# Kernel tuning notes

Hardware: AMD Instinct MI355X
Metric: run time of the kernel (lower is better)

The kernel has to match this reference:

```python
import jax, jax.numpy as jnp
import numpy as np

B, H, W, C = 16, 32, 32, 512
HEADS, DHEAD = 8, 64  # head * channel == C
GROUPS, EPS = 32, 1e-5


def setup_inputs() -> dict:
    key = jax.random.key(0)
    ks = jax.random.split(key, 6)
    return {
        "x": jax.random.normal(ks[0], (B, H, W, C), jnp.float32),
        "gn_gamma": jnp.ones((C,), jnp.float32),
        "gn_beta": jnp.zeros((C,), jnp.float32),
        "wq": jax.random.normal(ks[1], (C, HEADS * DHEAD), jnp.float32) * 0.02,
        "wk": jax.random.normal(ks[2], (C, HEADS * DHEAD), jnp.float32) * 0.02,
        "wv": jax.random.normal(ks[3], (C, HEADS * DHEAD), jnp.float32) * 0.02,
        "conv_w": jax.random.normal(ks[4], (3, 3, HEADS * DHEAD, C), jnp.float32) * 0.02,
        "conv_b": jnp.zeros((C,), jnp.float32),
    }


def _group_norm(x, gamma, beta):
    b, h, w, c = x.shape
    xg = x.reshape(b, h, w, GROUPS, c // GROUPS)
    mean = jnp.mean(xg, axis=(1, 2, 4), keepdims=True)
    var = jnp.var(xg, axis=(1, 2, 4), keepdims=True)
    xn = (xg - mean) * jax.lax.rsqrt(var + EPS)
    return xn.reshape(b, h, w, c) * gamma + beta


def reference(x, gn_gamma, gn_beta, wq, wk, wv, conv_w, conv_b):
    xn = _group_norm(x, gn_gamma, gn_beta)          # [B,H,W,C]
    t = xn.reshape(B, H * W, C)                      # tokens [B,S,C]
    q = (t @ wq).reshape(B, H * W, HEADS, DHEAD)
    k = (t @ wk).reshape(B, H * W, HEADS, DHEAD)
    v = (t @ wv).reshape(B, H * W, HEADS, DHEAD)
    scale = 1.0 / jnp.sqrt(jnp.asarray(DHEAD, q.dtype))
    scores = jnp.einsum("bqhd,bkhd->bhqk", q, k) * scale  # [B,HEADS,S,S]
    weights = jax.nn.softmax(scores, axis=-1)
    out = jnp.einsum("bhqk,bkhd->bqhd", weights, v)       # [B,S,HEADS,DHEAD]
    out = out.reshape(B, H, W, HEADS * DHEAD)
    y = jax.lax.conv_general_dilated(
        out, conv_w, window_strides=(1, 1), padding=((1, 1), (1, 1)),
        dimension_numbers=("NHWC", "HWIO", "NHWC")) + conv_b
    return y + x
```

## Files before the change

### kernel.cpp

```cpp
#include <hip/hip_runtime.h>
#include <hip/hip_bf16.h>

#define Bn 16
#define Cc 512
#define Ss 1024
#define HEADS 8
#define DHEAD 64
#define GROUPS 32
#define CPG 16
#define EPSv 1e-5f
#define Mtok (Bn*Ss)
#define QKVS 1536
#define QKS 1024
#define PROW 34
#define PIMG (PROW*PROW)

typedef __hip_bfloat16 bf16;
typedef __attribute__((ext_vector_type(8))) short short8;
typedef __attribute__((ext_vector_type(4))) float f32x4;

union U4 { uint4 u; bf16 h[8]; };
union B4 { ushort4 u; bf16 h[4]; };

__device__ __forceinline__ void stage16(const bf16* g, bf16* l) {
    __builtin_amdgcn_global_load_lds((const __attribute__((address_space(1))) void*)g,
                                     (__attribute__((address_space(3))) void*)l,
                                     16, 0, 0);
}

__device__ __forceinline__ unsigned int pkbf(float a, float b) {
    union { __hip_bfloat16 h; unsigned short u; } ua, ub;
    ua.h = __float2bfloat16(a); ub.h = __float2bfloat16(b);
    return ((unsigned int)ub.u << 16) | ua.u;
}

__device__ __forceinline__ void swz_decode(int F, int& r, int& c) {
    int line = F >> 3, pos = F & 7;
    int u = pos ^ (line & 7);
    r = (line << 1) | (u >> 2);
    c = u & 3;
}
__device__ __forceinline__ int swz_off(int r, int q) {
    return (r >> 1) * 64 + (((((r & 1) << 2) + q) ^ ((r >> 1) & 7)) << 3);
}

__global__ __launch_bounds__(256) void wtrans(const float* __restrict__ src,
                                              bf16* __restrict__ dst) {
    size_t off = (size_t)blockIdx.y * 262144;
    int t = blockIdx.x * 256 + threadIdx.x;
    int n = t & 511, k8 = (t >> 9) * 8;
    const float* s = src + off + (size_t)k8 * 512 + n;
    U4 o;
#pragma unroll
    for (int j = 0; j < 8; j++) o.h[j] = __float2bfloat16(s[(size_t)j * 512]);
    *(uint4*)(dst + off + (size_t)n * 512 + k8) = o.u;
}

__global__ __launch_bounds__(256) void gn_stats(const float* __restrict__ x,
                                                float* __restrict__ stats) {
    int bg = blockIdx.x;
    int b = bg >> 5, g = bg & 31;
    int tid = threadIdx.x;
    const size_t base = (size_t)b * Ss * Cc + g * CPG;
    float sum = 0.f, sq = 0.f;
    for (int i = tid; i < 4096; i += 256) {
        int s = i >> 2, c4 = (i & 3) * 4;
        float4 t = *(const float4*)(x + base + (size_t)s * Cc + c4);
        sum += t.x + t.y + t.z + t.w;
        sq  += t.x * t.x + t.y * t.y + t.z * t.z + t.w * t.w;
    }
    __shared__ float s1[4], s2[4];
#pragma unroll
    for (int off = 32; off > 0; off >>= 1) {
        sum += __shfl_down(sum, off);
        sq  += __shfl_down(sq,  off);
    }
    if ((tid & 63) == 0) { s1[tid >> 6] = sum; s2[tid >> 6] = sq; }
    __syncthreads();
    if (tid == 0) {
        float S = s1[0] + s1[1] + s1[2] + s1[3];
        float Q = s2[0] + s2[1] + s2[2] + s2[3];
        float mean = S * (1.f / 16384.f);
        float var  = Q * (1.f / 16384.f) - mean * mean;
        stats[bg * 2 + 0] = mean;
        stats[bg * 2 + 1] = rsqrtf(var + EPSv);
    }
}

__global__ __launch_bounds__(256) void gn_apply(const float* __restrict__ x,
                                                const float* __restrict__ stats,
                                                const float* __restrict__ gamma,
                                                const float* __restrict__ beta,
                                                bf16* __restrict__ xn) {
    size_t i = (size_t)blockIdx.x * 256 + threadIdx.x;
    size_t e = i * 4;
    int c0 = (int)(e & (Cc - 1));
    int token = (int)(e >> 9);
    int b = token >> 10;
    int g = c0 >> 4;
    float mean = stats[(b * 32 + g) * 2 + 0];
    float rstd = stats[(b * 32 + g) * 2 + 1];
    float4 t  = *(const float4*)(x + e);
    float4 gm = *(const float4*)(gamma + c0);
    float4 bt = *(const float4*)(beta + c0);
    B4 o;
    o.h[0] = __float2bfloat16((t.x - mean) * rstd * gm.x + bt.x);
    o.h[1] = __float2bfloat16((t.y - mean) * rstd * gm.y + bt.y);
    o.h[2] = __float2bfloat16((t.z - mean) * rstd * gm.z + bt.z);
    o.h[3] = __float2bfloat16((t.w - mean) * rstd * gm.w + bt.w);
    *(ushort4*)(xn + e) = o.u;
}

__global__ __launch_bounds__(256) void zero_pad(bf16* __restrict__ Pad) {
    int idx = blockIdx.x * 256 + threadIdx.x;
    int b = idx / (132 * 64);
    int rem = idx - b * 132 * 64;
    int t = rem >> 6, seg = rem & 63;
    int r, c;
    if (t < 34)      { r = 0;  c = t; }
    else if (t < 68) { r = 33; c = t - 34; }
    else { int u = t - 68; r = 1 + (u >> 1); c = (u & 1) * 33; }
    uint4 z = {0u, 0u, 0u, 0u};
    *(uint4*)(Pad + ((size_t)b * PIMG + r * PROW + c) * Cc + seg * 8) = z;
}

__global__ __launch_bounds__(256) void gemm_qkv(const bf16* __restrict__ A,
                                                const bf16* __restrict__ Wt,
                                                bf16* __restrict__ C,
                                                bf16* __restrict__ vT) {
    __shared__ __align__(16) bf16 As[128][32];
    __shared__ __align__(16) bf16 Bs[128][32];
    int tid = threadIdx.x;
    int wave = tid >> 6, lane = tid & 63;
    int l15 = lane & 15, quad = lane >> 4;
    int wm = wave >> 1, wn = wave & 1;
    int m0 = blockIdx.y * 128, n0 = blockIdx.x * 128;
    int lr = lane >> 2, kseg = (lane & 3) * 8;
    int ar0 = wave * 32 + lr;

    const bf16* ga = A  + (size_t)(m0 + ar0) * Cc + kseg;
    const bf16* gb = Wt + (size_t)(n0 + ar0) * Cc + kseg;
    bf16* la0 = &As[wave * 32][0];
    bf16* la1 = &As[wave * 32 + 16][0];
    bf16* lb0 = &Bs[wave * 32][0];
    bf16* lb1 = &Bs[wave * 32 + 16][0];

    f32x4 acc[4][4] = {};
    for (int k0 = 0; k0 < 512; k0 += 32) {
        __syncthreads();
        stage16(ga + k0,                  la0);
        stage16(ga + k0 + (size_t)16 * Cc, la1);
        stage16(gb + k0,                  lb0);
        stage16(gb + k0 + (size_t)16 * Cc, lb1);
        __syncthreads();
        short8 af[4], bfv[4];
#pragma unroll
        for (int mt = 0; mt < 4; mt++) af[mt]  = *(const short8*)&As[wm * 64 + mt * 16 + l15][quad * 8];
#pragma unroll
        for (int nt = 0; nt < 4; nt++) bfv[nt] = *(const short8*)&Bs[wn * 64 + nt * 16 + l15][quad * 8];
#pragma unroll
        for (int mt = 0; mt < 4; mt++)
#pragma unroll
            for (int nt = 0; nt < 4; nt++)
                acc[mt][nt] = __builtin_amdgcn_mfma_f32_16x16x32_bf16(af[mt], bfv[nt], acc[mt][nt], 0, 0, 0);
    }

    if (n0 < 1024) {
#pragma unroll
        for (int mt = 0; mt < 4; mt++)
#pragma unroll
            for (int r = 0; r < 4; r++) {
                size_t row = (size_t)(m0 + wm * 64 + mt * 16 + quad * 4 + r) * QKS + n0 + wn * 64 + l15;
#pragma unroll
                for (int nt = 0; nt < 4; nt++)
                    C[row + nt * 16] = __float2bfloat16(acc[mt][nt][r]);
            }
    } else {
        int hh = ((n0 - 1024) >> 6) + wn;
        int bq = m0 >> 10;
        int tok0 = (m0 & 1023) + wm * 64;
#pragma unroll
        for (int nt = 0; nt < 4; nt++) {
            int d = nt * 16 + l15;
            bf16* drow = vT + (size_t)(hh * 64 + d) * 16384 + bq * 1024 + tok0;
#pragma unroll
            for (int mt = 0; mt < 4; mt++) {
                B4 o;
#pragma unroll
                for (int r = 0; r < 4; r++) o.h[r] = __float2bfloat16(acc[mt][nt][r]);
                *(ushort4*)(drow + mt * 16 + quad * 4) = o.u;
            }
        }
    }
}

__global__ __launch_bounds__(256) void attention_mfma(const bf16* __restrict__ QK,
                                                      const bf16* __restrict__ vT,
                                                      bf16* __restrict__ Pad) {
    int blk = blockIdx.x;
    int qt = blk & 15;
    int bh = blk >> 4;
    int h = bh & (HEADS - 1), b = bh >> 3;
    int tid = threadIdx.x;
    int wave = tid >> 6, lane = tid & 63;
    int l15 = lane & 15, quad = lane >> 4;

    __shared__ __align__(16) bf16 KT[2][4096];
    __shared__ __align__(16) bf16 VTs[2][4096];

    const size_t base = (size_t)b * Ss * QKS + h * DHEAD;
    const bf16* kbase = QK + base + 512;

    int q0 = qt * 64 + wave * 16;
    const bf16* qrow = QK + base + (size_t)(q0 + l15) * QKS + quad * 8;
    short8 qf0 = *(const short8*)(qrow);
    short8 qf1 = *(const short8*)(qrow + 32);

    int r1 = tid >> 3,         f1 = (tid & 7) ^ (r1 & 7);
    int r2 = (tid + 256) >> 3, f2 = ((tid + 256) & 7) ^ (r2 & 7);
    const bf16* gk1 = kbase + (size_t)r1 * QKS + f1 * 8;
    const bf16* gk2 = kbase + (size_t)r2 * QKS + f2 * 8;
    const bf16* gv1 = vT + (size_t)(h * 64 + r1) * 16384 + b * 1024 + f1 * 8;
    const bf16* gv2 = vT + (size_t)(h * 64 + r2) * 16384 + b * 1024 + f2 * 8;

    f32x4 oaccT[4] = {{0.f,0.f,0.f,0.f},{0.f,0.f,0.f,0.f},{0.f,0.f,0.f,0.f},{0.f,0.f,0.f,0.f}};
    float lsum = 0.f;
    const f32x4 zero4 = {0.f, 0.f, 0.f, 0.f};
    int srcA = ((quad & 1) * 2) * 16 + l15;
    int srcB = srcA + 16;
    bool hiq = (quad >= 2);
    int sw = l15 & 7;

    auto stage = [&](int c0, int p) {
        stage16(gk1 + (size_t)c0 * QKS, &KT[p][wave * 512]);
        stage16(gk2 + (size_t)c0 * QKS, &KT[p][2048 + wave * 512]);
        stage16(gv1 + c0,               &VTs[p][wave * 512]);
        stage16(gv2 + c0,               &VTs[p][2048 + wave * 512]);
    };

    stage(0, 0);
    for (int it = 0; it < 16; ++it) {
        int p = it & 1;
        if (it + 1 < 16) {
            stage((it + 1) * 64, p ^ 1);
            asm volatile("s_waitcnt vmcnt(4)" ::: "memory");
        } else {
            asm volatile("s_waitcnt vmcnt(0)" ::: "memory");
        }
        __builtin_amdgcn_s_barrier();
        __builtin_amdgcn_sched_barrier(0);

        unsigned int pk[4][2];
        __builtin_amdgcn_s_setprio(1);
#pragma unroll
        for (int kb = 0; kb < 4; kb++) {
            const bf16* kr = &KT[p][(kb * 16 + l15) * 64];
            short8 kf0 = *(const short8*)(kr + ((quad ^ sw) * 8));
            short8 kf1 = *(const short8*)(kr + (((4 + quad) ^ sw) * 8));
            f32x4 s = __builtin_amdgcn_mfma_f32_16x16x32_bf16(kf0, qf0, zero4, 0, 0, 0);
            s = __builtin_amdgcn_mfma_f32_16x16x32_bf16(kf1, qf1, s, 0, 0, 0);
            float p0 = __expf(s[0] * 0.125f);
            float p1 = __expf(s[1] * 0.125f);
            float p2 = __expf(s[2] * 0.125f);
            float p3 = __expf(s[3] * 0.125f);
            lsum += (p0 + p1) + (p2 + p3);
            pk[kb][0] = pkbf(p0, p1);
            pk[kb][1] = pkbf(p2, p3);
        }
        __builtin_amdgcn_s_setprio(0);

        union { short8 s8; unsigned int u[4]; } PT0, PT1;
        {
            unsigned int A0 = __shfl((int)pk[0][0], srcA), A1 = __shfl((int)pk[0][1], srcA);
            unsigned int A2 = __shfl((int)pk[1][0], srcA), A3 = __shfl((int)pk[1][1], srcA);
            unsigned int B0 = __shfl((int)pk[0][0], srcB), B1 = __shfl((int)pk[0][1], srcB);
            unsigned int B2 = __shfl((int)pk[1][0], srcB), B3 = __shfl((int)pk[1][1], srcB);
            PT0.u[0] = hiq ? A2 : A0;  PT0.u[1] = hiq ? A3 : A1;
            PT0.u[2] = hiq ? B2 : B0;  PT0.u[3] = hiq ? B3 : B1;
            unsigned int C0 = __shfl((int)pk[2][0], srcA), C1 = __shfl((int)pk[2][1], srcA);
            unsigned int C2 = __shfl((int)pk[3][0], srcA), C3 = __shfl((int)pk[3][1], srcA);
            unsigned int D0 = __shfl((int)pk[2][0], srcB), D1 = __shfl((int)pk[2][1], srcB);
            unsigned int D2 = __shfl((int)pk[3][0], srcB), D3 = __shfl((int)pk[3][1], srcB);
            PT1.u[0] = hiq ? C2 : C0;  PT1.u[1] = hiq ? C3 : C1;
            PT1.u[2] = hiq ? D2 : D0;  PT1.u[3] = hiq ? D3 : D1;
        }

        __builtin_amdgcn_s_setprio(1);
#pragma unroll
        for (int dt = 0; dt < 4; dt++) {
            const bf16* vr = &VTs[p][(dt * 16 + l15) * 64];
            short8 vf0 = *(const short8*)(vr + ((quad ^ sw) * 8));
            short8 vf1 = *(const short8*)(vr + (((4 + quad) ^ sw) * 8));
            oaccT[dt] = __builtin_amdgcn_mfma_f32_16x16x32_bf16(vf0, PT0.s8, oaccT[dt], 0, 0, 0);
            oaccT[dt] = __builtin_amdgcn_mfma_f32_16x16x32_bf16(vf1, PT1.s8, oaccT[dt], 0, 0, 0);
        }
        __builtin_amdgcn_s_setprio(0);

        __builtin_amdgcn_sched_barrier(0);
        __builtin_amdgcn_s_barrier();
        __builtin_amdgcn_sched_barrier(0);
    }

    lsum += __shfl_xor(lsum, 16);
    lsum += __shfl_xor(lsum, 32);
    float inv = 1.f / lsum;

    int s = q0 + l15;
    size_t rowoff = ((size_t)(b * PROW + (s >> 5) + 1) * PROW + (s & 31) + 1) * Cc + h * DHEAD;
#pragma unroll
    for (int dt = 0; dt < 4; dt++) {
        B4 o;
#pragma unroll
        for (int r = 0; r < 4; r++) o.h[r] = __float2bfloat16(oaccT[dt][r] * inv);
        *(ushort4*)(Pad + rowoff + dt * 16 + quad * 4) = o.u;
    }
}

__global__ __launch_bounds__(256, 2) void conv_mfma(const bf16* __restrict__ Pad,
                                                    const bf16* __restrict__ Wct,
                                                    const float* __restrict__ bias,
                                                    const float* __restrict__ xres,
                                                    float* __restrict__ out) {
    __shared__ __align__(16) bf16 As[2][136 * 32];
    __shared__ __align__(16) bf16 Bs[2][3 * 4096];

    int tid = threadIdx.x;
    int wave = tid >> 6, lane = tid & 63;
    int l15 = lane & 15, quad = lane >> 4;
    int wm = wave >> 1, wn = wave & 1;
    int m0 = blockIdx.y * 128, n0 = blockIdx.x * 128;
    int b = m0 >> 10, oh0 = (m0 & 1023) >> 5;

    int rA1, cA1, rA2, cA2, rA3, cA3;
    swz_decode(tid,              rA1, cA1);
    swz_decode(tid + 256,        rA2, cA2);
    swz_decode((tid & 31) + 512, rA3, cA3);
    int rr1 = rA1 / 34, co1 = rA1 - rr1 * 34;
    int rr2 = rA2 / 34, co2 = rA2 - rr2 * 34;
    int rr3 = rA3 / 34, co3 = rA3 - rr3 * 34;
    const size_t dyStride = (size_t)PROW * Cc;
    const bf16* pA1 = Pad + ((size_t)b * PIMG + (size_t)(oh0 + rr1) * PROW + co1) * Cc + cA1 * 8;
    const bf16* pA2 = Pad + ((size_t)b * PIMG + (size_t)(oh0 + rr2) * PROW + co2) * Cc + cA2 * 8;
    const bf16* pA3 = Pad + ((size_t)b * PIMG + (size_t)(oh0 + rr3) * PROW + co3) * Cc + cA3 * 8;

    int rB1, cB1, rB2, cB2;
    swz_decode(wave * 128 + lane,      rB1, cB1);
    swz_decode(wave * 128 + 64 + lane, rB2, cB2);
    const bf16* gw1 = Wct + (size_t)(n0 + rB1) * Cc + cB1 * 8;
    const bf16* gw2 = Wct + (size_t)(n0 + rB2) * Cc + cB2 * 8;

    int aoff[3][4], boff[4];
#pragma unroll
    for (int mt = 0; mt < 4; mt++) {
        int rbase = (wm * 2 + (mt >> 1)) * 34 + (mt & 1) * 16 + l15;
#pragma unroll
        for (int dxi = 0; dxi < 3; dxi++) aoff[dxi][mt] = swz_off(rbase + dxi, quad);
    }
#pragma unroll
    for (int nt = 0; nt < 4; nt++) boff[nt] = swz_off(wn * 64 + nt * 16 + l15, quad);

    auto stage_it = [&](int it, int p) {
        int dyi = it >> 4;
        int k0 = (it & 15) << 5;
        size_t ag = (size_t)dyi * dyStride + k0;
        stage16(pA1 + ag, &As[p][wave * 512]);
        stage16(pA2 + ag, &As[p][2048 + wave * 512]);
        if (tid < 32) stage16(pA3 + ag, &As[p][4096]);
        size_t wg = (size_t)(dyi * 3) * (Cc * Cc) + k0;
#pragma unroll
        for (int t = 0; t < 3; t++) {
            size_t tg = wg + (size_t)t * (Cc * Cc);
            stage16(gw1 + tg, &Bs[p][t * 4096 + wave * 1024]);
            stage16(gw2 + tg, &Bs[p][t * 4096 + wave * 1024 + 512]);
        }
    };

    f32x4 acc[4][4] = {};
    stage_it(0, 0);
    for (int it = 0; it < 48; ++it) {
        int p = it & 1;
        if (it + 1 < 48) {
            stage_it(it + 1, p ^ 1);
            asm volatile("s_waitcnt vmcnt(8)" ::: "memory");
        } else {
            asm volatile("s_waitcnt vmcnt(0)" ::: "memory");
        }
        __builtin_amdgcn_s_barrier();

        short8 af[3][4], bfv[3][4];
#pragma unroll
        for (int dxi = 0; dxi < 3; dxi++) {
#pragma unroll
            for (int mt = 0; mt < 4; mt++)
                af[dxi][mt] = *(const short8*)&As[p][aoff[dxi][mt]];
#pragma unroll
            for (int nt = 0; nt < 4; nt++)
                bfv[dxi][nt] = *(const short8*)&Bs[p][dxi * 4096 + boff[nt]];
        }
        asm volatile("s_waitcnt lgkmcnt(0)" ::: "memory");
        __builtin_amdgcn_sched_barrier(0);
        __builtin_amdgcn_s_barrier();

#pragma unroll
        for (int dxi = 0; dxi < 3; dxi++)
#pragma unroll
            for (int mt = 0; mt < 4; mt++)
#pragma unroll
                for (int nt = 0; nt < 4; nt++)
                    acc[mt][nt] = __builtin_amdgcn_mfma_f32_16x16x32_bf16(af[dxi][mt], bfv[dxi][nt], acc[mt][nt], 0, 0, 0);
    }

#pragma unroll
    for (int mt = 0; mt < 4; mt++)
#pragma unroll
        for (int r = 0; r < 4; r++) {
            size_t row = (size_t)(m0 + wm * 64 + mt * 16 + quad * 4 + r) * Cc + n0 + wn * 64 + l15;
#pragma unroll
            for (int nt = 0; nt < 4; nt++) {
                int n = n0 + wn * 64 + nt * 16 + l15;
                out[row + nt * 16] = acc[mt][nt][r] + bias[n] + xres[row + nt * 16];
            }
        }
}

extern "C" void kernel_launch(void* const* d_in, const int* in_sizes, int n_in,
                              void* d_out, int out_size, void* d_ws, size_t ws_size,
                              hipStream_t stream) {
    const float* x     = (const float*)d_in[0];
    const float* gamma = (const float*)d_in[1];
    const float* beta  = (const float*)d_in[2];
    const float* wq    = (const float*)d_in[3];
    const float* wk    = (const float*)d_in[4];
    const float* wv    = (const float*)d_in[5];
    const float* convw = (const float*)d_in[6];
    const float* convb = (const float*)d_in[7];
    float* out = (float*)d_out;

    char* ws = (char*)d_ws;
    bf16*  pad   = (bf16*)ws;
    float* stats = (float*)ws;
    bf16*  xn    = (bf16*)(ws + 4096);
    bf16*  wt    = (bf16*)(ws + 4096 + ((size_t)16 << 20));
    bf16*  qk    = (bf16*)(ws + ((size_t)19 << 20));
    bf16*  vt    = (bf16*)(ws + ((size_t)51 << 20));
    bf16*  wct   = (bf16*)(ws + ((size_t)67 << 20));

    wtrans<<<dim3(128, 1), 256, 0, stream>>>(wq, wt);
    wtrans<<<dim3(128, 1), 256, 0, stream>>>(wk, wt + 262144);
    wtrans<<<dim3(128, 1), 256, 0, stream>>>(wv, wt + 524288);
    wtrans<<<dim3(128, 9), 256, 0, stream>>>(convw, wct);

    gn_stats<<<dim3(Bn * GROUPS), 256, 0, stream>>>(x, stats);
    gn_apply<<<dim3(Mtok * Cc / (4 * 256)), 256, 0, stream>>>(x, stats, gamma, beta, xn);

    gemm_qkv<<<dim3(QKVS / 128, Mtok / 128), 256, 0, stream>>>(xn, wt, qk, vt);

    zero_pad<<<dim3(528), 256, 0, stream>>>(pad);
    attention_mfma<<<dim3(Bn * HEADS * (Ss / 64)), 256, 0, stream>>>(qk, vt, pad);

    conv_mfma<<<dim3(Cc / 128, Mtok / 128), 256, 0, stream>>>(pad, wct, convb, x, out);
}
```

Measured before the change: 316.5 us.

## Process two 16-row query tiles per wave in attention to reuse K/V

Each attention block now covers 128 queries instead of 64, with each wave handling two 16-query sub-tiles that share the same K and V fragments loaded from LDS. This halves the number of blocks and the global K/V staging traffic per query, and doubles MFMA work per LDS read. The cost is more registers for the doubled accumulators and packed probabilities, and fewer blocks (1024), which may reduce occupancy and latency hiding.

```diff
diff --git a/kernel.cpp b/kernel.cpp
--- a/kernel.cpp
+++ b/kernel.cpp
@@ -198,8 +198,8 @@
                                                       const bf16* __restrict__ vT,
                                                       bf16* __restrict__ Pad) {
     int blk = blockIdx.x;
-    int qt = blk & 15;
-    int bh = blk >> 4;
+    int qt = blk & 7;
+    int bh = blk >> 3;
     int h = bh & (HEADS - 1), b = bh >> 3;
     int tid = threadIdx.x;
     int wave = tid >> 6, lane = tid & 63;
@@ -211,10 +211,12 @@
     const size_t base = (size_t)b * Ss * QKS + h * DHEAD;
     const bf16* kbase = QK + base + 512;
 
-    int q0 = qt * 64 + wave * 16;
+    int q0 = qt * 128 + wave * 32;
     const bf16* qrow = QK + base + (size_t)(q0 + l15) * QKS + quad * 8;
-    short8 qf0 = *(const short8*)(qrow);
-    short8 qf1 = *(const short8*)(qrow + 32);
+    short8 qfA0 = *(const short8*)(qrow);
+    short8 qfA1 = *(const short8*)(qrow + 32);
+    short8 qfB0 = *(const short8*)(qrow + 16 * QKS);
+    short8 qfB1 = *(const short8*)(qrow + 16 * QKS + 32);
 
     int r1 = tid >> 3,         f1 = (tid & 7) ^ (r1 & 7);
     int r2 = (tid + 256) >> 3, f2 = ((tid + 256) & 7) ^ (r2 & 7);
@@ -223,8 +225,9 @@
     const bf16* gv1 = vT + (size_t)(h * 64 + r1) * 16384 + b * 1024 + f1 * 8;
     const bf16* gv2 = vT + (size_t)(h * 64 + r2) * 16384 + b * 1024 + f2 * 8;
 
-    f32x4 oaccT[4] = {{0.f,0.f,0.f,0.f},{0.f,0.f,0.f,0.f},{0.f,0.f,0.f,0.f},{0.f,0.f,0.f,0.f}};
-    float lsum = 0.f;
+    f32x4 oacc0[4] = {{0.f,0.f,0.f,0.f},{0.f,0.f,0.f,0.f},{0.f,0.f,0.f,0.f},{0.f,0.f,0.f,0.f}};
+    f32x4 oacc1[4] = {{0.f,0.f,0.f,0.f},{0.f,0.f,0.f,0.f},{0.f,0.f,0.f,0.f},{0.f,0.f,0.f,0.f}};
+    float lsum0 = 0.f, lsum1 = 0.f;
     const f32x4 zero4 = {0.f, 0.f, 0.f, 0.f};
     int srcA = ((quad & 1) * 2) * 16 + l15;
     int srcB = srcA + 16;
@@ -250,39 +253,62 @@
         __builtin_amdgcn_s_barrier();
         __builtin_amdgcn_sched_barrier(0);
 
-        unsigned int pk[4][2];
+        unsigned int pk0[4][2], pk1[4][2];
         __builtin_amdgcn_s_setprio(1);
 #pragma unroll
         for (int kb = 0; kb < 4; kb++) {
             const bf16* kr = &KT[p][(kb * 16 + l15) * 64];
             short8 kf0 = *(const short8*)(kr + ((quad ^ sw) * 8));
             short8 kf1 = *(const short8*)(kr + (((4 + quad) ^ sw) * 8));
-            f32x4 s = __builtin_amdgcn_mfma_f32_16x16x32_bf16(kf0, qf0, zero4, 0, 0, 0);
-            s = __builtin_amdgcn_mfma_f32_16x16x32_bf16(kf1, qf1, s, 0, 0, 0);
-            float p0 = __expf(s[0] * 0.125f);
-            float p1 = __expf(s[1] * 0.125f);
-            float p2 = __expf(s[2] * 0.125f);
-            float p3 = __expf(s[3] * 0.125f);
-            lsum += (p0 + p1) + (p2 + p3);
-            pk[kb][0] = pkbf(p0, p1);
-            pk[kb][1] = pkbf(p2, p3);
+            f32x4 s0 = __builtin_amdgcn_mfma_f32_16x16x32_bf16(kf0, qfA0, zero4, 0, 0, 0);
+            s0 = __builtin_amdgcn_mfma_f32_16x16x32_bf16(kf1, qfA1, s0, 0, 0, 0);
+            f32x4 s1 = __builtin_amdgcn_mfma_f32_16x16x32_bf16(kf0, qfB0, zero4, 0, 0, 0);
+            s1 = __builtin_amdgcn_mfma_f32_16x16x32_bf16(kf1, qfB1, s1, 0, 0, 0);
+            float a0 = __expf(s0[0] * 0.125f);
+            float a1 = __expf(s0[1] * 0.125f);
+            float a2 = __expf(s0[2] * 0.125f);
+            float a3 = __expf(s0[3] * 0.125f);
+            lsum0 += (a0 + a1) + (a2 + a3);
+            pk0[kb][0] = pkbf(a0, a1);
+            pk0[kb][1] = pkbf(a2, a3);
+            float b0 = __expf(s1[0] * 0.125f);
+            float b1 = __expf(s1[1] * 0.125f);
+            float b2 = __expf(s1[2] * 0.125f);
+            float b3 = __expf(s1[3] * 0.125f);
+            lsum1 += (b0 + b1) + (b2 + b3);
+            pk1[kb][0] = pkbf(b0, b1);
+            pk1[kb][1] = pkbf(b2, b3);
         }
         __builtin_amdgcn_s_setprio(0);
 
-        union { short8 s8; unsigned int u[4]; } PT0, PT1;
+        union { short8 s8; unsigned int u[4]; } PT00, PT01, PT10, PT11;
         {
-            unsigned int A0 = __shfl((int)pk[0][0], srcA), A1 = __shfl((int)pk[0][1], srcA);
-            unsigned int A2 = __shfl((int)pk[1][0], srcA), A3 = __shfl((int)pk[1][1], srcA);
-            unsigned int B0 = __shfl((int)pk[0][0], srcB), B1 = __shfl((int)pk[0][1], srcB);
-            unsigned int B2 = __shfl((int)pk[1][0], srcB), B3 = __shfl((int)pk[1][1], srcB);
-            PT0.u[0] = hiq ? A2 : A0;  PT0.u[1] = hiq ? A3 : A1;
-            PT0.u[2] = hiq ? B2 : B0;  PT0.u[3] = hiq ? B3 : B1;
-            unsigned int C0 = __shfl((int)pk[2][0], srcA), C1 = __shfl((int)pk[2][1], srcA);
-            unsigned int C2 = __shfl((int)pk[3][0], srcA), C3 = __shfl((int)pk[3][1], srcA);
-            unsigned int D0 = __shfl((int)pk[2][0], srcB), D1 = __shfl((int)pk[2][1], srcB);
-            unsigned int D2 = __shfl((int)pk[3][0], srcB), D3 = __shfl((int)pk[3][1], srcB);
-            PT1.u[0] = hiq ? C2 : C0;  PT1.u[1] = hiq ? C3 : C1;
-            PT1.u[2] = hiq ? D2 : D0;  PT1.u[3] = hiq ? D3 : D1;
+            unsigned int A0 = __shfl((int)pk0[0][0], srcA), A1 = __shfl((int)pk0[0][1], srcA);
+            unsigned int A2 = __shfl((int)pk0[1][0], srcA), A3 = __shfl((int)pk0[1][1], srcA);
+            unsigned int B0 = __shfl((int)pk0[0][0], srcB), B1 = __shfl((int)pk0[0][1], srcB);
+            unsigned int B2 = __shfl((int)pk0[1][0], srcB), B3 = __shfl((int)pk0[1][1], srcB);
+            PT00.u[0] = hiq ? A2 : A0;  PT00.u[1] = hiq ? A3 : A1;
+            PT00.u[2] = hiq ? B2 : B0;  PT00.u[3] = hiq ? B3 : B1;
+            unsigned int C0 = __shfl((int)pk0[2][0], srcA), C1 = __shfl((int)pk0[2][1], srcA);
+            unsigned int C2 = __shfl((int)pk0[3][0], srcA), C3 = __shfl((int)pk0[3][1], srcA);
+            unsigned int D0 = __shfl((int)pk0[2][0], srcB), D1 = __shfl((int)pk0[2][1], srcB);
+            unsigned int D2 = __shfl((int)pk0[3][0], srcB), D3 = __shfl((int)pk0[3][1], srcB);
+            PT01.u[0] = hiq ? C2 : C0;  PT01.u[1] = hiq ? C3 : C1;
+            PT01.u[2] = hiq ? D2 : D0;  PT01.u[3] = hiq ? D3 : D1;
+        }
+        {
+            unsigned int A0 = __shfl((int)pk1[0][0], srcA), A1 = __shfl((int)pk1[0][1], srcA);
+            unsigned int A2 = __shfl((int)pk1[1][0], srcA), A3 = __shfl((int)pk1[1][1], srcA);
+            unsigned int B0 = __shfl((int)pk1[0][0], srcB), B1 = __shfl((int)pk1[0][1], srcB);
+            unsigned int B2 = __shfl((int)pk1[1][0], srcB), B3 = __shfl((int)pk1[1][1], srcB);
+            PT10.u[0] = hiq ? A2 : A0;  PT10.u[1] = hiq ? A3 : A1;
+            PT10.u[2] = hiq ? B2 : B0;  PT10.u[3] = hiq ? B3 : B1;
+            unsigned int C0 = __shfl((int)pk1[2][0], srcA), C1 = __shfl((int)pk1[2][1], srcA);
+            unsigned int C2 = __shfl((int)pk1[3][0], srcA), C3 = __shfl((int)pk1[3][1], srcA);
+            unsigned int D0 = __shfl((int)pk1[2][0], srcB), D1 = __shfl((int)pk1[2][1], srcB);
+            unsigned int D2 = __shfl((int)pk1[3][0], srcB), D3 = __shfl((int)pk1[3][1], srcB);
+            PT11.u[0] = hiq ? C2 : C0;  PT11.u[1] = hiq ? C3 : C1;
+            PT11.u[2] = hiq ? D2 : D0;  PT11.u[3] = hiq ? D3 : D1;
         }
 
         __builtin_amdgcn_s_setprio(1);
@@ -291,8 +317,10 @@
             const bf16* vr = &VTs[p][(dt * 16 + l15) * 64];
             short8 vf0 = *(const short8*)(vr + ((quad ^ sw) * 8));
             short8 vf1 = *(const short8*)(vr + (((4 + quad) ^ sw) * 8));
-            oaccT[dt] = __builtin_amdgcn_mfma_f32_16x16x32_bf16(vf0, PT0.s8, oaccT[dt], 0, 0, 0);
-            oaccT[dt] = __builtin_amdgcn_mfma_f32_16x16x32_bf16(vf1, PT1.s8, oaccT[dt], 0, 0, 0);
+            oacc0[dt] = __builtin_amdgcn_mfma_f32_16x16x32_bf16(vf0, PT00.s8, oacc0[dt], 0, 0, 0);
+            oacc0[dt] = __builtin_amdgcn_mfma_f32_16x16x32_bf16(vf1, PT01.s8, oacc0[dt], 0, 0, 0);
+            oacc1[dt] = __builtin_amdgcn_mfma_f32_16x16x32_bf16(vf0, PT10.s8, oacc1[dt], 0, 0, 0);
+            oacc1[dt] = __builtin_amdgcn_mfma_f32_16x16x32_bf16(vf1, PT11.s8, oacc1[dt], 0, 0, 0);
         }
         __builtin_amdgcn_s_setprio(0);
 
@@ -301,18 +329,34 @@
         __builtin_amdgcn_sched_barrier(0);
     }
 
-    lsum += __shfl_xor(lsum, 16);
-    lsum += __shfl_xor(lsum, 32);
-    float inv = 1.f / lsum;
-
-    int s = q0 + l15;
-    size_t rowoff = ((size_t)(b * PROW + (s >> 5) + 1) * PROW + (s & 31) + 1) * Cc + h * DHEAD;
-#pragma unroll
-    for (int dt = 0; dt < 4; dt++) {
-        B4 o;
-#pragma unroll
-        for (int r = 0; r < 4; r++) o.h[r] = __float2bfloat16(oaccT[dt][r] * inv);
-        *(ushort4*)(Pad + rowoff + dt * 16 + quad * 4) = o.u;
+    lsum0 += __shfl_xor(lsum0, 16);
+    lsum0 += __shfl_xor(lsum0, 32);
+    lsum1 += __shfl_xor(lsum1, 16);
+    lsum1 += __shfl_xor(lsum1, 32);
+    float inv0 = 1.f / lsum0;
+    float inv1 = 1.f / lsum1;
+
+    {
+        int s = q0 + l15;
+        size_t rowoff = ((size_t)(b * PROW + (s >> 5) + 1) * PROW + (s & 31) + 1) * Cc + h * DHEAD;
+#pragma unroll
+        for (int dt = 0; dt < 4; dt++) {
+            B4 o;
+#pragma unroll
+            for (int r = 0; r < 4; r++) o.h[r] = __float2bfloat16(oacc0[dt][r] * inv0);
+            *(ushort4*)(Pad + rowoff + dt * 16 + quad * 4) = o.u;
+        }
+    }
+    {
+        int s = q0 + 16 + l15;
+        size_t rowoff = ((size_t)(b * PROW + (s >> 5) + 1) * PROW + (s & 31) + 1) * Cc + h * DHEAD;
+#pragma unroll
+        for (int dt = 0; dt < 4; dt++) {
+            B4 o;
+#pragma unroll
+            for (int r = 0; r < 4; r++) o.h[r] = __float2bfloat16(oacc1[dt][r] * inv1);
+            *(ushort4*)(Pad + rowoff + dt * 16 + quad * 4) = o.u;
+        }
     }
 }
 
@@ -456,7 +500,7 @@
     gemm_qkv<<<dim3(QKVS / 128, Mtok / 128), 256, 0, stream>>>(xn, wt, qk, vt);
 
     zero_pad<<<dim3(528), 256, 0, stream>>>(pad);
-    attention_mfma<<<dim3(Bn * HEADS * (Ss / 64)), 256, 0, stream>>>(qk, vt, pad);
+    attention_mfma<<<dim3(Bn * HEADS * (Ss / 128)), 256, 0, stream>>>(qk, vt, pad);
 
     conv_mfma<<<dim3(Cc / 128, Mtok / 128), 256, 0, stream>>>(pad, wct, convb, x, out);
 }
```

New measurement: 319.0 us. No clear change (+0.8%).
